# Optimization experiments

Hardware: AMD Instinct MI355X
Metric: run time of the kernel (lower is better)

The kernel has to match this reference:

```python
import jax, jax.numpy as jnp
import numpy as np

NUM_ROUTES = 1152
NUM_CAPS = 10
CAPS_IN = 8
CAPS_DIM = 16
BATCH = 128
NUM_IT = 3


def _squash(s):
    # s: [..., caps_dim]; scale = |s|^2 / ((1+|s|^2) * |s|)
    sqn = jnp.sum(s * s, axis=-1, keepdims=True)
    return s * (sqn / ((1.0 + sqn) * jnp.sqrt(sqn)))


def setup_inputs() -> dict:
    key = jax.random.key(0)
    k1, k2 = jax.random.split(key)
    x = jax.random.normal(k1, (BATCH, NUM_ROUTES, CAPS_IN), dtype=jnp.float32)
    W = jax.random.normal(k2, (1, NUM_ROUTES, NUM_CAPS, CAPS_DIM, CAPS_IN), dtype=jnp.float32)
    return {"input": x, "W": W}


def reference(input, W):
    # u_hat[b,r,j,d] = W[r,j,d,c] @ x[b,r,c]  (original broadcasts W over batch)
    u_hat = jnp.einsum('rjdc,brc->brjd', W[0], input)
    r, j = u_hat.shape[1], u_hat.shape[2]
    b_ij = jnp.zeros((r, j), dtype=u_hat.dtype)  # shared across batch, as in original
    v = None
    for _ in range(NUM_IT):
        c_ij = jax.nn.softmax(b_ij, axis=1)          # softmax over num_caps (dim=2 orig)
        s = jnp.einsum('rj,brjd->bjd', c_ij, u_hat)  # weighted sum over routes
        v = _squash(s)                                # [bs, num_caps, caps_dim]
        # agreement: <u_hat, v> averaged over batch (original updates every iter)
        b_ij = b_ij + jnp.mean(jnp.einsum('brjd,bjd->brj', u_hat, v), axis=0)
    return v[..., None]  # [bs, num_caps, caps_dim, 1], matches v_j.squeeze(1) shape
```

## Files before the change

kernel.cpp:

```cpp
#include <hip/hip_runtime.h>
#include <math.h>

#define R_ROUTES 1152
#define N_CAPS 10
#define C_IN 8
#define D_DIM 16
#define B_BATCH 128
#define JD 160
#define KK 9216
#define KSPLIT 48
#define RS 24
#define NG 5
#define BH 2
#define SPART 20480

typedef __attribute__((ext_vector_type(8))) short short8;
typedef __attribute__((ext_vector_type(4))) float f32x4;

__device__ inline unsigned short f2bf(float f) {
    unsigned int u = __float_as_uint(f);
    unsigned int r = u + 0x7FFFu + ((u >> 16) & 1u);
    return (unsigned short)(r >> 16);
}
__device__ inline float bf2f(unsigned short h) {
    return __uint_as_float(((unsigned int)h) << 16);
}


__global__ __launch_bounds__(256) void k_prep0(
    const float* __restrict__ x, unsigned short* __restrict__ xT,
    f32x4* __restrict__ zbase) {
    __shared__ float tile[32][33];
    int id = blockIdx.x, t = threadIdx.x;
    if (id < 288) {
        int bx = id;
        int tx = t & 31, ty = t >> 5;
        for (int by = 0; by < 4; by++) {
            if (by) __syncthreads();
#pragma unroll
            for (int i = 0; i < 4; i++) {
                int row = ty + i * 8;
                tile[row][tx] = x[(size_t)(by * 32 + row) * KK + bx * 32 + tx];
            }
            __syncthreads();
#pragma unroll
            for (int i = 0; i < 4; i++) {
                int row = ty + i * 8;
                xT[(size_t)(bx * 32 + row) * B_BATCH + by * 32 + tx] = f2bf(tile[tx][row]);
            }
        }
        return;
    }
    int idx = (id - 288) * 256 + t;
    zbase[idx] = (f32x4){0.f, 0.f, 0.f, 0.f};
}

template <int FIRST, int STORE>
__global__ __launch_bounds__(256) void k_iter(
    const float* __restrict__ x, const float* __restrict__ W,
    const float* __restrict__ ctab, float* __restrict__ s) {
    int t = threadIdx.x;
    int ks = blockIdx.x, ng = blockIdx.y, bh = blockIdx.z;
    int r0 = ks * RS, jd0 = ng * 32, b_base = bh * 64;
    int w = t >> 6, l = t & 63, row = l & 15, quad = l >> 4;
    const float* px = x + (size_t)(b_base + w * 16 + row) * KK + ks * 192;
    f32x4 acc0 = {0,0,0,0}, acc1 = {0,0,0,0};
#pragma unroll
    for (int st = 0; st < 6; st++) {
        int rr = r0 + st * 4 + quad;
        float c0 = FIRST ? 0.1f : ctab[rr * N_CAPS + (jd0 >> 4)];
        float c1 = FIRST ? 0.1f : ctab[rr * N_CAPS + (jd0 >> 4) + 1];
        const float4* wp0 = (const float4*)(W + ((size_t)rr * JD + jd0 + row) * C_IN);
        const float4* wp1 = (const float4*)(W + ((size_t)rr * JD + jd0 + 16 + row) * C_IN);
        float4 wa = wp0[0], wb = wp0[1], wc = wp1[0], wd = wp1[1];
        float wv0[8] = {wa.x,wa.y,wa.z,wa.w, wb.x,wb.y,wb.z,wb.w};
        float wv1[8] = {wc.x,wc.y,wc.z,wc.w, wd.x,wd.y,wd.z,wd.w};
        short8 Bh0, Bh1;
#pragma unroll
        for (int i = 0; i < 8; i++) {
            Bh0[i] = (short)f2bf(wv0[i] * c0);
            Bh1[i] = (short)f2bf(wv1[i] * c1);
        }
        float4 x0 = *(const float4*)(px + st * 32 + quad * 8);
        float4 x1 = *(const float4*)(px + st * 32 + quad * 8 + 4);
        float xv[8] = {x0.x,x0.y,x0.z,x0.w, x1.x,x1.y,x1.z,x1.w};
        short8 Ah, Al;
#pragma unroll
        for (int i = 0; i < 8; i++) {
            unsigned short h = f2bf(xv[i]);
            Ah[i] = (short)h;
            Al[i] = (short)f2bf(xv[i] - bf2f(h));
        }
        acc0 = __builtin_amdgcn_mfma_f32_16x16x32_bf16(Ah, Bh0, acc0, 0, 0, 0);
        acc0 = __builtin_amdgcn_mfma_f32_16x16x32_bf16(Al, Bh0, acc0, 0, 0, 0);
        acc1 = __builtin_amdgcn_mfma_f32_16x16x32_bf16(Ah, Bh1, acc1, 0, 0, 0);
        acc1 = __builtin_amdgcn_mfma_f32_16x16x32_bf16(Al, Bh1, acc1, 0, 0, 0);
    }
    if (STORE) {
        float* sp = s + (size_t)ks * SPART;
#pragma unroll
        for (int i = 0; i < 4; i++) {
            int b0 = b_base + w * 16 + quad * 4 + i;
            sp[(size_t)b0 * JD + jd0 + row]      = acc0[i];
            sp[(size_t)b0 * JD + jd0 + 16 + row] = acc1[i];
        }
    } else {
#pragma unroll
        for (int i = 0; i < 4; i++) {
            int b0 = b_base + w * 16 + quad * 4 + i;
            atomicAdd(&s[(size_t)b0 * JD + jd0 + row],      acc0[i]);
            atomicAdd(&s[(size_t)b0 * JD + jd0 + 16 + row], acc1[i]);
        }
    }
}

template <int ACCUM>
__global__ __launch_bounds__(256) void k_va(
    const unsigned short* __restrict__ xT, const float* __restrict__ s_prev,
    const float* __restrict__ W, float* __restrict__ b_ij,
    float* __restrict__ ctab) {
    __shared__ unsigned short vb[JD][136];
    __shared__ float bnew[4][N_CAPS];
    int t = threadIdx.x;
    int r0 = blockIdx.x * 4, rc0 = blockIdx.x * 32;

#pragma unroll
    for (int q = 0; q < 5; q++) {
        int pi = t * 5 + q;
        int b = pi / N_CAPS, j = pi % N_CAPS;
        const float4* sp4 = (const float4*)(s_prev + (size_t)b * JD + j * D_DIM);
        float4 a0 = sp4[0], a1 = sp4[1], a2 = sp4[2], a3 = sp4[3];
        float sv[D_DIM] = {a0.x,a0.y,a0.z,a0.w, a1.x,a1.y,a1.z,a1.w,
                           a2.x,a2.y,a2.z,a2.w, a3.x,a3.y,a3.z,a3.w};
        float sqn = 0.f;
#pragma unroll
        for (int d = 0; d < D_DIM; d++) sqn = fmaf(sv[d], sv[d], sqn);
        float scale = sqn / ((1.f + sqn) * sqrtf(sqn));
#pragma unroll
        for (int d = 0; d < D_DIM; d++)
            vb[j * D_DIM + d][b] = f2bf(sv[d] * scale);
    }
    __syncthreads();

    int w = t >> 6, l = t & 63, row = l & 15, quad = l >> 4;
    int rhalf = l >> 5, cbase = (quad & 1) * 4;

#pragma unroll
    for (int jt = 0; jt < 5; jt++) {
        int u = jt * 4 + w;
        int mt = u / 10, nt = u % 10;
        const short8* pa = (const short8*)(xT + (size_t)(rc0 + mt * 16 + row) * B_BATCH);
        f32x4 acc = {0,0,0,0};
#pragma unroll
        for (int st = 0; st < 4; st++)
            acc = __builtin_amdgcn_mfma_f32_16x16x32_bf16(
                pa[st * 4 + quad],
                *(const short8*)&vb[nt * 16 + row][st * 32 + quad * 8],
                acc, 0, 0, 0);
        int r = r0 + 2 * mt + rhalf;
        const float* wp = W + ((size_t)r * JD + nt * 16 + row) * C_IN + cbase;
        float4 w4 = *(const float4*)wp;
        float part = acc[0]*w4.x + acc[1]*w4.y + acc[2]*w4.z + acc[3]*w4.w;
#pragma unroll
        for (int off = 1; off < 32; off <<= 1) part += __shfl_xor(part, off, 32);
        if ((l & 31) == 0) bnew[2 * mt + rhalf][nt] = part * (1.f / (float)B_BATCH);
    }
    __syncthreads();

    if (t < 4) {
        float bj[N_CAPS], m = -1e30f;
#pragma unroll
        for (int j = 0; j < N_CAPS; j++) {
            float base = ACCUM ? b_ij[(r0 + t) * N_CAPS + j] : 0.f;
            bj[j] = base + bnew[t][j];
            m = fmaxf(m, bj[j]);
        }
        if (!ACCUM) {
#pragma unroll
            for (int j = 0; j < N_CAPS; j++) b_ij[(r0 + t) * N_CAPS + j] = bj[j];
        }
        float sum = 0.f;
#pragma unroll
        for (int j = 0; j < N_CAPS; j++) { bj[j] = expf(bj[j] - m); sum += bj[j]; }
        float inv = 1.f / sum;
#pragma unroll
        for (int j = 0; j < N_CAPS; j++) ctab[(r0 + t) * N_CAPS + j] = bj[j] * inv;
    }
}

__global__ __launch_bounds__(320) void k_final(
    const float* __restrict__ s2p, float* __restrict__ out) {
    int t = threadIdx.x;
    int bloc = t / JD, jd = t % JD;
    int b = blockIdx.x * 2 + bloc;
    float acc = 0.f;
#pragma unroll
    for (int ks = 0; ks < KSPLIT; ks++)
        acc += s2p[(size_t)ks * SPART + (size_t)b * JD + jd];
    float sq = acc * acc;
#pragma unroll
    for (int off = 1; off < 16; off <<= 1) sq += __shfl_xor(sq, off, 16);
    float scale = sq / ((1.f + sq) * sqrtf(sq));
    out[(size_t)b * JD + jd] = acc * scale;
}

extern "C" void kernel_launch(void* const* d_in, const int* in_sizes, int n_in,
                              void* d_out, int out_size, void* d_ws, size_t ws_size,
                              hipStream_t stream) {
    const float* x = (const float*)d_in[0];
    const float* W = (const float*)d_in[1];
    float* out = (float*)d_out;
    char* ws = (char*)d_ws;

    float*          s0   = (float*)(ws + 0);
    float*          s1   = (float*)(ws + 81920);
    float*          b_ij = (float*)(ws + 163840);
    float*          ctab = (float*)(ws + 209920);
    unsigned short* xT   = (unsigned short*)(ws + 256000);
    float*          s2p  = (float*)(ws + 2615296);

    k_prep0<<<328, 256, 0, stream>>>(x, xT, (f32x4*)ws);

    k_iter<1, 0><<<dim3(KSPLIT, NG, BH), 256, 0, stream>>>(x, W, nullptr, s0);

    k_va<0><<<288, 256, 0, stream>>>(xT, s0, W, b_ij, ctab);

    k_iter<0, 0><<<dim3(KSPLIT, NG, BH), 256, 0, stream>>>(x, W, ctab, s1);

    k_va<1><<<288, 256, 0, stream>>>(xT, s1, W, b_ij, ctab);

    k_iter<0, 1><<<dim3(KSPLIT, NG, BH), 256, 0, stream>>>(x, W, ctab, s2p);

    k_final<<<64, 320, 0, stream>>>(s2p, out);
}
```

Baseline: 112.0 us.

## Replace split-K atomics with full-K blocks reducing in shared memory

Result: slower. 175.6 us (+56.9%).

```diff
diff --git a/kernel.cpp b/kernel.cpp
--- a/kernel.cpp
+++ b/kernel.cpp
@@ -8,11 +8,11 @@
 #define B_BATCH 128
 #define JD 160
 #define KK 9216
-#define KSPLIT 48
-#define RS 24
-#define NG 5
-#define BH 2
-#define SPART 20480
+#define JG 10
+#define BS 8
+#define NW 8
+#define KW 1152
+#define NST 36
 
 typedef __attribute__((ext_vector_type(8))) short short8;
 typedef __attribute__((ext_vector_type(4))) float f32x4;
@@ -27,63 +27,29 @@
 }
 
 
-__global__ __launch_bounds__(256) void k_prep0(
-    const float* __restrict__ x, unsigned short* __restrict__ xT,
-    f32x4* __restrict__ zbase) {
-    __shared__ float tile[32][33];
-    int id = blockIdx.x, t = threadIdx.x;
-    if (id < 288) {
-        int bx = id;
-        int tx = t & 31, ty = t >> 5;
-        for (int by = 0; by < 4; by++) {
-            if (by) __syncthreads();
-#pragma unroll
-            for (int i = 0; i < 4; i++) {
-                int row = ty + i * 8;
-                tile[row][tx] = x[(size_t)(by * 32 + row) * KK + bx * 32 + tx];
-            }
-            __syncthreads();
-#pragma unroll
-            for (int i = 0; i < 4; i++) {
-                int row = ty + i * 8;
-                xT[(size_t)(bx * 32 + row) * B_BATCH + by * 32 + tx] = f2bf(tile[tx][row]);
-            }
-        }
-        return;
-    }
-    int idx = (id - 288) * 256 + t;
-    zbase[idx] = (f32x4){0.f, 0.f, 0.f, 0.f};
-}
-
-template <int FIRST, int STORE>
-__global__ __launch_bounds__(256) void k_iter(
+template <int FIRST, int FINAL>
+__device__ inline void full_body(
     const float* __restrict__ x, const float* __restrict__ W,
-    const float* __restrict__ ctab, float* __restrict__ s) {
-    int t = threadIdx.x;
-    int ks = blockIdx.x, ng = blockIdx.y, bh = blockIdx.z;
-    int r0 = ks * RS, jd0 = ng * 32, b_base = bh * 64;
-    int w = t >> 6, l = t & 63, row = l & 15, quad = l >> 4;
-    const float* px = x + (size_t)(b_base + w * 16 + row) * KK + ks * 192;
-    f32x4 acc0 = {0,0,0,0}, acc1 = {0,0,0,0};
-#pragma unroll
-    for (int st = 0; st < 6; st++) {
-        int rr = r0 + st * 4 + quad;
-        float c0 = FIRST ? 0.1f : ctab[rr * N_CAPS + (jd0 >> 4)];
-        float c1 = FIRST ? 0.1f : ctab[rr * N_CAPS + (jd0 >> 4) + 1];
-        const float4* wp0 = (const float4*)(W + ((size_t)rr * JD + jd0 + row) * C_IN);
-        const float4* wp1 = (const float4*)(W + ((size_t)rr * JD + jd0 + 16 + row) * C_IN);
-        float4 wa = wp0[0], wb = wp0[1], wc = wp1[0], wd = wp1[1];
-        float wv0[8] = {wa.x,wa.y,wa.z,wa.w, wb.x,wb.y,wb.z,wb.w};
-        float wv1[8] = {wc.x,wc.y,wc.z,wc.w, wd.x,wd.y,wd.z,wd.w};
-        short8 Bh0, Bh1;
-#pragma unroll
-        for (int i = 0; i < 8; i++) {
-            Bh0[i] = (short)f2bf(wv0[i] * c0);
-            Bh1[i] = (short)f2bf(wv1[i] * c1);
-        }
+    const float* __restrict__ ctab, float* __restrict__ dst,
+    f32x4 (*__restrict__ red)[64], int jg, int bs, int t) {
+    int jd0 = jg * 16, b0 = bs * 16;
+    int ww = t >> 6, l = t & 63, row = l & 15, quad = l >> 4;
+    const float* px = x + (size_t)(b0 + row) * KK + ww * KW;
+    int rbase = ww * (KW / C_IN);
+    f32x4 acc = {0, 0, 0, 0};
+#pragma unroll 4
+    for (int st = 0; st < NST; st++) {
+        int rr = rbase + st * 4 + quad;
+        float c0 = FIRST ? 0.1f : ctab[rr * N_CAPS + jg];
+        const float4* wp = (const float4*)(W + ((size_t)rr * JD + jd0 + row) * C_IN);
+        float4 wa = wp[0], wb = wp[1];
+        float wv[8] = {wa.x, wa.y, wa.z, wa.w, wb.x, wb.y, wb.z, wb.w};
+        short8 Bh;
+#pragma unroll
+        for (int i = 0; i < 8; i++) Bh[i] = (short)f2bf(wv[i] * c0);
         float4 x0 = *(const float4*)(px + st * 32 + quad * 8);
         float4 x1 = *(const float4*)(px + st * 32 + quad * 8 + 4);
-        float xv[8] = {x0.x,x0.y,x0.z,x0.w, x1.x,x1.y,x1.z,x1.w};
+        float xv[8] = {x0.x, x0.y, x0.z, x0.w, x1.x, x1.y, x1.z, x1.w};
         short8 Ah, Al;
 #pragma unroll
         for (int i = 0; i < 8; i++) {
@@ -91,27 +57,69 @@
             Ah[i] = (short)h;
             Al[i] = (short)f2bf(xv[i] - bf2f(h));
         }
-        acc0 = __builtin_amdgcn_mfma_f32_16x16x32_bf16(Ah, Bh0, acc0, 0, 0, 0);
-        acc0 = __builtin_amdgcn_mfma_f32_16x16x32_bf16(Al, Bh0, acc0, 0, 0, 0);
-        acc1 = __builtin_amdgcn_mfma_f32_16x16x32_bf16(Ah, Bh1, acc1, 0, 0, 0);
-        acc1 = __builtin_amdgcn_mfma_f32_16x16x32_bf16(Al, Bh1, acc1, 0, 0, 0);
-    }
-    if (STORE) {
-        float* sp = s + (size_t)ks * SPART;
+        acc = __builtin_amdgcn_mfma_f32_16x16x32_bf16(Ah, Bh, acc, 0, 0, 0);
+        acc = __builtin_amdgcn_mfma_f32_16x16x32_bf16(Al, Bh, acc, 0, 0, 0);
+    }
+    if (ww > 0) red[ww - 1][l] = acc;
+    __syncthreads();
+    if (ww == 0) {
+#pragma unroll
+        for (int j = 0; j < NW - 1; j++) {
+            f32x4 r = red[j][l];
+            acc[0] += r[0]; acc[1] += r[1]; acc[2] += r[2]; acc[3] += r[3];
+        }
+        if (FINAL) {
+#pragma unroll
+            for (int i = 0; i < 4; i++) {
+                float v = acc[i], sq = v * v;
+#pragma unroll
+                for (int off = 1; off < 16; off <<= 1) sq += __shfl_xor(sq, off, 16);
+                float scale = sq / ((1.f + sq) * sqrtf(sq));
+                dst[(size_t)(b0 + quad * 4 + i) * JD + jd0 + row] = v * scale;
+            }
+        } else {
+#pragma unroll
+            for (int i = 0; i < 4; i++)
+                dst[(size_t)(b0 + quad * 4 + i) * JD + jd0 + row] = acc[i];
+        }
+    }
+}
+
+__global__ __launch_bounds__(512) void k_head(
+    const float* __restrict__ x, const float* __restrict__ W,
+    unsigned short* __restrict__ xT, float* __restrict__ s0) {
+    __shared__ f32x4 red[NW - 1][64];
+    __shared__ float tile[2][32][33];
+    int id = blockIdx.x, t = threadIdx.x;
+    if (id < JG * BS) {
+        full_body<1, 0>(x, W, nullptr, s0, red, id % JG, id / JG, t);
+        return;
+    }
+    int sub = t >> 8, tt = t & 255;
+    int bx = (id - JG * BS) * 2 + sub;
+    int tx = tt & 31, ty = tt >> 5;
+    for (int by = 0; by < 4; by++) {
+        if (by) __syncthreads();
 #pragma unroll
         for (int i = 0; i < 4; i++) {
-            int b0 = b_base + w * 16 + quad * 4 + i;
-            sp[(size_t)b0 * JD + jd0 + row]      = acc0[i];
-            sp[(size_t)b0 * JD + jd0 + 16 + row] = acc1[i];
-        }
-    } else {
+            int row = ty + i * 8;
+            tile[sub][row][tx] = x[(size_t)(by * 32 + row) * KK + bx * 32 + tx];
+        }
+        __syncthreads();
 #pragma unroll
         for (int i = 0; i < 4; i++) {
-            int b0 = b_base + w * 16 + quad * 4 + i;
-            atomicAdd(&s[(size_t)b0 * JD + jd0 + row],      acc0[i]);
-            atomicAdd(&s[(size_t)b0 * JD + jd0 + 16 + row], acc1[i]);
-        }
-    }
+            int row = ty + i * 8;
+            xT[(size_t)(bx * 32 + row) * B_BATCH + by * 32 + tx] = f2bf(tile[sub][tx][row]);
+        }
+    }
+}
+
+template <int FINAL>
+__global__ __launch_bounds__(512) void k_full(
+    const float* __restrict__ x, const float* __restrict__ W,
+    const float* __restrict__ ctab, float* __restrict__ dst) {
+    __shared__ f32x4 red[NW - 1][64];
+    full_body<0, FINAL>(x, W, ctab, dst, red, blockIdx.x, blockIdx.y, threadIdx.x);
 }
 
 template <int ACCUM>
@@ -150,7 +158,7 @@
         int u = jt * 4 + w;
         int mt = u / 10, nt = u % 10;
         const short8* pa = (const short8*)(xT + (size_t)(rc0 + mt * 16 + row) * B_BATCH);
-        f32x4 acc = {0,0,0,0};
+        f32x4 acc = {0, 0, 0, 0};
 #pragma unroll
         for (int st = 0; st < 4; st++)
             acc = __builtin_amdgcn_mfma_f32_16x16x32_bf16(
@@ -188,22 +196,6 @@
     }
 }
 
-__global__ __launch_bounds__(320) void k_final(
-    const float* __restrict__ s2p, float* __restrict__ out) {
-    int t = threadIdx.x;
-    int bloc = t / JD, jd = t % JD;
-    int b = blockIdx.x * 2 + bloc;
-    float acc = 0.f;
-#pragma unroll
-    for (int ks = 0; ks < KSPLIT; ks++)
-        acc += s2p[(size_t)ks * SPART + (size_t)b * JD + jd];
-    float sq = acc * acc;
-#pragma unroll
-    for (int off = 1; off < 16; off <<= 1) sq += __shfl_xor(sq, off, 16);
-    float scale = sq / ((1.f + sq) * sqrtf(sq));
-    out[(size_t)b * JD + jd] = acc * scale;
-}
-
 extern "C" void kernel_launch(void* const* d_in, const int* in_sizes, int n_in,
                               void* d_out, int out_size, void* d_ws, size_t ws_size,
                               hipStream_t stream) {
@@ -217,19 +209,14 @@
     float*          b_ij = (float*)(ws + 163840);
     float*          ctab = (float*)(ws + 209920);
     unsigned short* xT   = (unsigned short*)(ws + 256000);
-    float*          s2p  = (float*)(ws + 2615296);
-
-    k_prep0<<<328, 256, 0, stream>>>(x, xT, (f32x4*)ws);
-
-    k_iter<1, 0><<<dim3(KSPLIT, NG, BH), 256, 0, stream>>>(x, W, nullptr, s0);
+
+    k_head<<<JG * BS + 144, 512, 0, stream>>>(x, W, xT, s0);
 
     k_va<0><<<288, 256, 0, stream>>>(xT, s0, W, b_ij, ctab);
 
-    k_iter<0, 0><<<dim3(KSPLIT, NG, BH), 256, 0, stream>>>(x, W, ctab, s1);
+    k_full<0><<<dim3(JG, BS), 512, 0, stream>>>(x, W, ctab, s1);
 
     k_va<1><<<288, 256, 0, stream>>>(xT, s1, W, b_ij, ctab);
 
-    k_iter<0, 1><<<dim3(KSPLIT, NG, BH), 256, 0, stream>>>(x, W, ctab, s2p);
-
-    k_final<<<64, 320, 0, stream>>>(s2p, out);
-}
+    k_full<1><<<dim3(JG, BS), 512, 0, stream>>>(x, W, ctab, out);
+}
```
